# Kernel tuning notes

Measured on AMD Instinct MI355X. Metric: run time of the kernel, lower is better.

The kernel has to match this reference:

```python
import jax, jax.numpy as jnp
import numpy as np

L, D, H = 4, 1024, 16
HD = D // H
VOCAB = 100000
EPS = 1e-5


def layernorm(x, g, b):
    mu = jnp.mean(x, axis=-1, keepdims=True)
    var = jnp.var(x, axis=-1, keepdims=True)
    return (x - mu) * jax.lax.rsqrt(var + EPS) * g + b


def setup_inputs() -> dict:
    key = jax.random.key(0)
    ks = jax.random.split(key, 12)
    s = 0.02
    return {
        "input_ids": jax.random.randint(ks[0], (8, 512), 0, VOCAB),
        "encoder_state": jax.random.normal(ks[1], (8, 1024, D), dtype=jnp.float32),
        "cross_attn_mask": jnp.zeros((8, 1, 1, 1024), dtype=jnp.float32),
        "emb": jax.random.normal(ks[2], (VOCAB, D), dtype=jnp.float32) * s,
        "ln_g": jnp.ones((L, D), dtype=jnp.float32),
        "ln_b": jnp.zeros((L, D), dtype=jnp.float32),
        "wq": jax.random.normal(ks[3], (L, D, D), dtype=jnp.float32) * s,
        "bq": jnp.zeros((L, D), dtype=jnp.float32),
        "wk": jax.random.normal(ks[4], (L, D, D), dtype=jnp.float32) * s,
        "bk": jnp.zeros((L, D), dtype=jnp.float32),
        "wv": jax.random.normal(ks[5], (L, D, D), dtype=jnp.float32) * s,
        "bv": jnp.zeros((L, D), dtype=jnp.float32),
    }


def reference(input_ids, encoder_state, cross_attn_mask, emb, ln_g, ln_b, wq, bq, wk, bk, wv, bv):
    N, Tq = input_ids.shape
    Tk = encoder_state.shape[1]
    scale = 1.0 / (HD ** 0.5)
    x = emb[input_ids]  # [N, Tq, D]; dropout is identity at eval
    for i in range(L):
        h = layernorm(x, ln_g[i], ln_b[i])
        q = (h @ wq[i] + bq[i]).reshape(N, Tq, H, HD)
        k = (encoder_state @ wk[i] + bk[i]).reshape(N, Tk, H, HD)
        v = (encoder_state @ wv[i] + bv[i]).reshape(N, Tk, H, HD)
        logits = jnp.einsum("bqhd,bkhd->bhqk", q, k) * scale + cross_attn_mask
        w = jax.nn.softmax(logits, axis=-1)
        x = jnp.einsum("bhqk,bkhd->bqhd", w, v).reshape(N, Tq, D)
        # note: no residual connection in the original layer
    return x
```

## Files before the change

### kernel.cpp

```cpp
#include <hip/hip_runtime.h>
#include <hip/hip_bf16.h>


typedef __attribute__((ext_vector_type(8))) short   bf16x8;
typedef __attribute__((ext_vector_type(8))) __bf16  bf16x8v;
typedef __attribute__((ext_vector_type(4))) short   s16x4;
typedef __attribute__((ext_vector_type(4))) float   f32x4;

__device__ inline short bf16s(float f) {
  __hip_bfloat16 h = __float2bfloat16(f);
  return *reinterpret_cast<short*>(&h);
}

__device__ inline f32x4 mfma16x16x32(bf16x8 a, bf16x8 b, f32x4 c) {
  return __builtin_amdgcn_mfma_f32_16x16x32_bf16(
      __builtin_bit_cast(bf16x8v, a), __builtin_bit_cast(bf16x8v, b), c, 0, 0, 0);
}

__global__ __launch_bounds__(256) void conv_bf16_kernel(const float* __restrict__ in,
                                                        short* __restrict__ out) {
  int i = (blockIdx.x * 256 + threadIdx.x) * 4;
  float4 v = *reinterpret_cast<const float4*>(in + i);
  s16x4 o; o.x = bf16s(v.x); o.y = bf16s(v.y); o.z = bf16s(v.z); o.w = bf16s(v.w);
  *reinterpret_cast<s16x4*>(out + i) = o;
}

__global__ __launch_bounds__(256) void transpose_w_kernel(
    const float* __restrict__ wq, const float* __restrict__ wk, const float* __restrict__ wv,
    short* __restrict__ wqT, short* __restrict__ wkvT) {
  int mat = blockIdx.z;
  const float* src; short* dst;
  if (mat < 4)      { src = wq + (long)mat * 1048576;       dst = wqT  + (long)mat * 1048576; }
  else if (mat < 8) { src = wk + (long)(mat - 4) * 1048576; dst = wkvT + (long)(mat - 4) * 2097152; }
  else              { src = wv + (long)(mat - 8) * 1048576; dst = wkvT + (long)(mat - 8) * 2097152 + 1048576; }
  __shared__ float t[32][33];
  int tx = threadIdx.x, ty = threadIdx.y;
  int x0 = blockIdx.x * 32, y0 = blockIdx.y * 32;
  #pragma unroll
  for (int j = 0; j < 32; j += 8)
    t[ty + j][tx] = src[(long)(y0 + ty + j) * 1024 + x0 + tx];
  __syncthreads();
  #pragma unroll
  for (int j = 0; j < 32; j += 8)
    dst[(long)(x0 + ty + j) * 1024 + y0 + tx] = bf16s(t[tx][ty + j]);
}

__global__ __launch_bounds__(256) void gather_kernel(const int* __restrict__ ids,
                                                     const float* __restrict__ emb,
                                                     float* __restrict__ x) {
  int row = blockIdx.x;
  long id = ids[row];
  float4 v = reinterpret_cast<const float4*>(emb + id * 1024)[threadIdx.x];
  reinterpret_cast<float4*>(x + (long)row * 1024)[threadIdx.x] = v;
}

__global__ __launch_bounds__(256) void ln_kernel(const float* __restrict__ x,
                                                 const float* __restrict__ g,
                                                 const float* __restrict__ b,
                                                 short* __restrict__ h) {
  int row = blockIdx.x, t = threadIdx.x;
  float4 v = reinterpret_cast<const float4*>(x + (long)row * 1024)[t];
  float s  = v.x + v.y + v.z + v.w;
  float sq = v.x * v.x + v.y * v.y + v.z * v.z + v.w * v.w;
  #pragma unroll
  for (int m = 32; m >= 1; m >>= 1) { s += __shfl_xor(s, m); sq += __shfl_xor(sq, m); }
  __shared__ float red[8];
  int w = t >> 6;
  if ((t & 63) == 0) { red[w * 2] = s; red[w * 2 + 1] = sq; }
  __syncthreads();
  s  = red[0] + red[2] + red[4] + red[6];
  sq = red[1] + red[3] + red[5] + red[7];
  float mu  = s * 0.0009765625f;
  float var = sq * 0.0009765625f - mu * mu;
  float rs  = rsqrtf(var + 1e-5f);
  float4 gg = reinterpret_cast<const float4*>(g)[t];
  float4 bb = reinterpret_cast<const float4*>(b)[t];
  s16x4 o;
  o.x = bf16s((v.x - mu) * rs * gg.x + bb.x);
  o.y = bf16s((v.y - mu) * rs * gg.y + bb.y);
  o.z = bf16s((v.z - mu) * rs * gg.z + bb.z);
  o.w = bf16s((v.w - mu) * rs * gg.w + bb.w);
  reinterpret_cast<s16x4*>(h + (long)row * 1024)[t] = o;
}

template <int KV>
__global__ __launch_bounds__(256, 2) void gemm_kernel(
    const short* __restrict__ A, const short* __restrict__ WT,
    const float* __restrict__ bias0, const float* __restrict__ bias1,
    short* __restrict__ out0, short* __restrict__ out1) {
  __shared__ union {
    struct { short a[128 * 64]; short b[128 * 64]; } s;
    short c[4][64 * 72];
  } lds;

  const int t = threadIdx.x;
  const int lane = t & 63, w = t >> 6;
  const int lo = lane & 15, hi = lane >> 4;
  const int wr = w >> 1, wc = w & 1;
  const long bm0 = (long)blockIdx.x * 128, bn0 = (long)blockIdx.y * 128;

  f32x4 acc[4][4] = {};

  const int srow = t >> 3;
  const int sc = t & 7;

  for (int kt = 0; kt < 16; ++kt) {
    __syncthreads();
    #pragma unroll
    for (int p = 0; p < 4; ++p) {
      const int row = p * 32 + srow;
      const int cs = sc ^ (row & 7);
      __builtin_amdgcn_global_load_lds(
          (const __attribute__((address_space(1))) void*)(A + (bm0 + row) * 1024 + kt * 64 + cs * 8),
          (__attribute__((address_space(3))) void*)&lds.s.a[row * 64 + sc * 8], 16, 0, 0);
      __builtin_amdgcn_global_load_lds(
          (const __attribute__((address_space(1))) void*)(WT + (bn0 + row) * 1024 + kt * 64 + cs * 8),
          (__attribute__((address_space(3))) void*)&lds.s.b[row * 64 + sc * 8], 16, 0, 0);
    }
    __syncthreads();
    #pragma unroll
    for (int kk = 0; kk < 2; ++kk) {
      bf16x8 af[4], bfr[4];
      #pragma unroll
      for (int i = 0; i < 4; ++i) {
        const int ar = wr * 64 + i * 16 + lo;
        af[i] = *reinterpret_cast<const bf16x8*>(
            &lds.s.a[ar * 64 + (((kk * 4 + hi) ^ (ar & 7)) * 8)]);
        const int br = wc * 64 + i * 16 + lo;
        bfr[i] = *reinterpret_cast<const bf16x8*>(
            &lds.s.b[br * 64 + (((kk * 4 + hi) ^ (br & 7)) * 8)]);
      }
      #pragma unroll
      for (int i = 0; i < 4; ++i)
        #pragma unroll
        for (int j = 0; j < 4; ++j)
          acc[i][j] = mfma16x16x32(af[i], bfr[j], acc[i][j]);
    }
  }

  const bool vpath = KV && (bn0 >= 1024);
  float bval[4];
  #pragma unroll
  for (int j = 0; j < 4; ++j) {
    const int col = (int)bn0 + wc * 64 + j * 16 + lo;
    bval[j] = vpath ? bias1[col - 1024] : bias0[col];
  }

  if (vpath) {
    const int bidx = (int)(bm0 >> 10);
    const int tk0  = (int)(bm0 & 1023);
    #pragma unroll
    for (int i = 0; i < 4; ++i) {
      const int tok = tk0 + wr * 64 + i * 16 + 4 * hi;
      #pragma unroll
      for (int j = 0; j < 4; ++j) {
        const int dfull = (int)bn0 - 1024 + wc * 64 + j * 16 + lo;
        s16x4 pk;
        #pragma unroll
        for (int r = 0; r < 4; ++r) pk[r] = bf16s(acc[i][j][r] + bval[j]);
        *reinterpret_cast<s16x4*>(out1 + ((long)(bidx * 1024 + dfull)) * 1024 + tok) = pk;
      }
    }
  } else {
    __syncthreads();
    #pragma unroll
    for (int i = 0; i < 4; ++i)
      #pragma unroll
      for (int j = 0; j < 4; ++j)
        #pragma unroll
        for (int r = 0; r < 4; ++r)
          lds.c[w][(i * 16 + 4 * hi + r) * 72 + j * 16 + lo] = bf16s(acc[i][j][r] + bval[j]);
    asm volatile("s_waitcnt lgkmcnt(0)" ::: "memory");
    #pragma unroll
    for (int ps = 0; ps < 8; ++ps) {
      const int rr = ps * 8 + (lane >> 3);
      const int cc = (lane & 7) * 8;
      bf16x8 vv = *reinterpret_cast<const bf16x8*>(&lds.c[w][rr * 72 + cc]);
      *reinterpret_cast<bf16x8*>(out0 + (bm0 + wr * 64 + rr) * 1024 + bn0 + wc * 64 + cc) = vv;
    }
  }
}

__global__ __launch_bounds__(256) void attn_kernel(
    const short* __restrict__ qbuf, const short* __restrict__ kbuf,
    const short* __restrict__ vT, const float* __restrict__ mask,
    float* __restrict__ dst) {
  __shared__ short pl[4][16 * 40];
  const int b = blockIdx.x >> 4, h = blockIdx.x & 15;
  const int t = threadIdx.x, w = t >> 6, lane = t & 63;
  const int lo = lane & 15, hi = lane >> 4;
  const int q0 = blockIdx.y * 64 + w * 16;

  const short* qrow = qbuf + (long)(b * 512 + q0 + lo) * 1024 + h * 64;
  const bf16x8 aq0 = *reinterpret_cast<const bf16x8*>(qrow + hi * 8);
  const bf16x8 aq1 = *reinterpret_cast<const bf16x8*>(qrow + 32 + hi * 8);

  f32x4 o[4] = {};
  float m_r[4] = {-1e30f, -1e30f, -1e30f, -1e30f};
  float l_r[4] = {};
  const float scale = 0.125f;
  const float* mrow = mask + b * 1024;
  short* plw = pl[w];

  for (int kb = 0; kb < 32; ++kb) {
    const short* kbase = kbuf + (long)(b * 1024 + kb * 32) * 1024 + h * 64;
    bf16x8 b00 = *reinterpret_cast<const bf16x8*>(kbase + (long)lo * 1024 + hi * 8);
    bf16x8 b01 = *reinterpret_cast<const bf16x8*>(kbase + (long)lo * 1024 + 32 + hi * 8);
    bf16x8 b10 = *reinterpret_cast<const bf16x8*>(kbase + (long)(16 + lo) * 1024 + hi * 8);
    bf16x8 b11 = *reinterpret_cast<const bf16x8*>(kbase + (long)(16 + lo) * 1024 + 32 + hi * 8);
    f32x4 z = {0.f, 0.f, 0.f, 0.f};
    f32x4 s0 = mfma16x16x32(aq0, b00, z);
    s0 = mfma16x16x32(aq1, b01, s0);
    f32x4 s1 = mfma16x16x32(aq0, b10, z);
    s1 = mfma16x16x32(aq1, b11, s1);

    const float mk0 = mrow[kb * 32 + lo];
    const float mk1 = mrow[kb * 32 + 16 + lo];

    float p0[4], p1[4], lm[4];
    #pragma unroll
    for (int r = 0; r < 4; ++r) {
      p0[r] = s0[r] * scale + mk0;
      p1[r] = s1[r] * scale + mk1;
      lm[r] = fmaxf(p0[r], p1[r]);
    }
    #pragma unroll
    for (int mm = 1; mm <= 8; mm <<= 1)
      #pragma unroll
      for (int r = 0; r < 4; ++r) lm[r] = fmaxf(lm[r], __shfl_xor(lm[r], mm));

    float alpha[4], ts[4];
    #pragma unroll
    for (int r = 0; r < 4; ++r) {
      const float mn = fmaxf(m_r[r], lm[r]);
      alpha[r] = __expf(m_r[r] - mn);
      m_r[r] = mn;
      p0[r] = __expf(p0[r] - mn);
      p1[r] = __expf(p1[r] - mn);
      ts[r] = p0[r] + p1[r];
    }
    #pragma unroll
    for (int mm = 1; mm <= 8; mm <<= 1)
      #pragma unroll
      for (int r = 0; r < 4; ++r) ts[r] += __shfl_xor(ts[r], mm);

    #pragma unroll
    for (int r = 0; r < 4; ++r) {
      l_r[r] = l_r[r] * alpha[r] + ts[r];
      o[0][r] *= alpha[r]; o[1][r] *= alpha[r]; o[2][r] *= alpha[r]; o[3][r] *= alpha[r];
      plw[(4 * hi + r) * 40 + lo]      = bf16s(p0[r]);
      plw[(4 * hi + r) * 40 + 16 + lo] = bf16s(p1[r]);
    }
    asm volatile("s_waitcnt lgkmcnt(0)" ::: "memory");
    const bf16x8 pa = *reinterpret_cast<const bf16x8*>(&plw[lo * 40 + hi * 8]);
    const short* vbase = vT + ((long)(b * 1024 + h * 64)) * 1024 + kb * 32;
    #pragma unroll
    for (int nd = 0; nd < 4; ++nd) {
      bf16x8 bv = *reinterpret_cast<const bf16x8*>(vbase + (long)(nd * 16 + lo) * 1024 + hi * 8);
      o[nd] = mfma16x16x32(pa, bv, o[nd]);
    }
  }

  #pragma unroll
  for (int r = 0; r < 4; ++r) {
    const float invl = 1.0f / l_r[r];
    float* drow = dst + (long)(b * 512 + q0 + 4 * hi + r) * 1024 + h * 64;
    #pragma unroll
    for (int nd = 0; nd < 4; ++nd) drow[nd * 16 + lo] = o[nd][r] * invl;
  }
}

extern "C" void kernel_launch(void* const* d_in, const int* in_sizes, int n_in,
                              void* d_out, int out_size, void* d_ws, size_t ws_size,
                              hipStream_t stream) {
  const int*   ids  = (const int*)d_in[0];
  const float* enc  = (const float*)d_in[1];
  const float* mask = (const float*)d_in[2];
  const float* emb  = (const float*)d_in[3];
  const float* ln_g = (const float*)d_in[4];
  const float* ln_b = (const float*)d_in[5];
  const float* wq   = (const float*)d_in[6];
  const float* bq   = (const float*)d_in[7];
  const float* wk   = (const float*)d_in[8];
  const float* bk   = (const float*)d_in[9];
  const float* wv   = (const float*)d_in[10];
  const float* bv   = (const float*)d_in[11];
  float* out = (float*)d_out;

  char* ws = (char*)d_ws;
  short* encB = (short*)ws; ws += (long)8192 * 1024 * 2;
  short* wqT  = (short*)ws; ws += (long)4 * 1024 * 1024 * 2;
  short* wkvT = (short*)ws; ws += (long)4 * 2048 * 1024 * 2;
  float* xbuf = (float*)ws; ws += (long)4096 * 1024 * 4;
  short* hbuf = (short*)ws; ws += (long)4096 * 1024 * 2;
  short* qbuf = (short*)ws; ws += (long)4096 * 1024 * 2;
  short* kbuf = (short*)ws; ws += (long)8192 * 1024 * 2;
  short* vT   = (short*)ws; ws += (long)8192 * 1024 * 2;

  conv_bf16_kernel<<<8192, 256, 0, stream>>>(enc, encB);
  transpose_w_kernel<<<dim3(32, 32, 12), dim3(32, 8), 0, stream>>>(wq, wk, wv, wqT, wkvT);
  gather_kernel<<<4096, 256, 0, stream>>>(ids, emb, xbuf);

  for (int i = 0; i < 4; ++i) {
    ln_kernel<<<4096, 256, 0, stream>>>(xbuf, ln_g + i * 1024, ln_b + i * 1024, hbuf);
    gemm_kernel<0><<<dim3(32, 8), 256, 0, stream>>>(
        hbuf, wqT + (long)i * 1024 * 1024, bq + i * 1024, nullptr, qbuf, nullptr);
    gemm_kernel<1><<<dim3(64, 16), 256, 0, stream>>>(
        encB, wkvT + (long)i * 2048 * 1024, bk + i * 1024, bv + i * 1024, kbuf, vT);
    float* dst = (i == 3) ? out : xbuf;
    attn_kernel<<<dim3(128, 8), 256, 0, stream>>>(qbuf, kbuf, vT, mask, dst);
  }
}
```

Baseline: 1.225 ms.

## Batch all-layer KV projections into one GEMM and widen attention key blocks

The K/V projections do not depend on the layer chain, so all four layers' K and V are now computed in a single large GEMM launch before the loop and kept in per-layer workspace buffers. The attention kernel processes 64 keys per iteration instead of 32, uses a swizzled LDS layout for the probability tile, and skips rescaling when the running max grows by 8 or less. MFMA sections are also wrapped in s_setprio. This removes three small GEMM launches and makes each one fill the GPU better, at the cost of four times the K/V workspace memory. The skipped rescale lets unnormalized exponentials reach up to e^8, which bf16 and fp32 can hold.

```diff
diff --git a/kernel.cpp b/kernel.cpp
--- a/kernel.cpp
+++ b/kernel.cpp
@@ -97,7 +97,11 @@
   const int lane = t & 63, w = t >> 6;
   const int lo = lane & 15, hi = lane >> 4;
   const int wr = w >> 1, wc = w & 1;
-  const long bm0 = (long)blockIdx.x * 128, bn0 = (long)blockIdx.y * 128;
+  const long bm0 = (long)blockIdx.x * 128;
+  const long bn0g = (long)blockIdx.y * 128;
+  const int  layer = KV ? (int)(bn0g >> 11) : 0;
+  const long bn0 = KV ? (bn0g & 2047) : bn0g;
+  const short* WTl = KV ? WT + (long)layer * 2097152 : WT;
 
   f32x4 acc[4][4] = {};
 
@@ -114,7 +118,7 @@
           (const __attribute__((address_space(1))) void*)(A + (bm0 + row) * 1024 + kt * 64 + cs * 8),
           (__attribute__((address_space(3))) void*)&lds.s.a[row * 64 + sc * 8], 16, 0, 0);
       __builtin_amdgcn_global_load_lds(
-          (const __attribute__((address_space(1))) void*)(WT + (bn0 + row) * 1024 + kt * 64 + cs * 8),
+          (const __attribute__((address_space(1))) void*)(WTl + (bn0 + row) * 1024 + kt * 64 + cs * 8),
           (__attribute__((address_space(3))) void*)&lds.s.b[row * 64 + sc * 8], 16, 0, 0);
     }
     __syncthreads();
@@ -130,11 +134,13 @@
         bfr[i] = *reinterpret_cast<const bf16x8*>(
             &lds.s.b[br * 64 + (((kk * 4 + hi) ^ (br & 7)) * 8)]);
       }
+      __builtin_amdgcn_s_setprio(1);
       #pragma unroll
       for (int i = 0; i < 4; ++i)
         #pragma unroll
         for (int j = 0; j < 4; ++j)
           acc[i][j] = mfma16x16x32(af[i], bfr[j], acc[i][j]);
+      __builtin_amdgcn_s_setprio(0);
     }
   }
 
@@ -143,8 +149,10 @@
   #pragma unroll
   for (int j = 0; j < 4; ++j) {
     const int col = (int)bn0 + wc * 64 + j * 16 + lo;
-    bval[j] = vpath ? bias1[col - 1024] : bias0[col];
-  }
+    bval[j] = KV ? (vpath ? bias1[layer * 1024 + col - 1024] : bias0[layer * 1024 + col])
+                 : bias0[col];
+  }
+  const long lofs = (long)layer * 8388608;
 
   if (vpath) {
     const int bidx = (int)(bm0 >> 10);
@@ -158,7 +166,7 @@
         s16x4 pk;
         #pragma unroll
         for (int r = 0; r < 4; ++r) pk[r] = bf16s(acc[i][j][r] + bval[j]);
-        *reinterpret_cast<s16x4*>(out1 + ((long)(bidx * 1024 + dfull)) * 1024 + tok) = pk;
+        *reinterpret_cast<s16x4*>(out1 + lofs + ((long)(bidx * 1024 + dfull)) * 1024 + tok) = pk;
       }
     }
   } else {
@@ -176,7 +184,7 @@
       const int rr = ps * 8 + (lane >> 3);
       const int cc = (lane & 7) * 8;
       bf16x8 vv = *reinterpret_cast<const bf16x8*>(&lds.c[w][rr * 72 + cc]);
-      *reinterpret_cast<bf16x8*>(out0 + (bm0 + wr * 64 + rr) * 1024 + bn0 + wc * 64 + cc) = vv;
+      *reinterpret_cast<bf16x8*>(out0 + lofs + (bm0 + wr * 64 + rr) * 1024 + bn0 + wc * 64 + cc) = vv;
     }
   }
 }
@@ -185,7 +193,7 @@
     const short* __restrict__ qbuf, const short* __restrict__ kbuf,
     const short* __restrict__ vT, const float* __restrict__ mask,
     float* __restrict__ dst) {
-  __shared__ short pl[4][16 * 40];
+  __shared__ short pl[4][16 * 64];
   const int b = blockIdx.x >> 4, h = blockIdx.x & 15;
   const int t = threadIdx.x, w = t >> 6, lane = t & 63;
   const int lo = lane & 15, hi = lane >> 4;
@@ -200,65 +208,93 @@
   float l_r[4] = {};
   const float scale = 0.125f;
   const float* mrow = mask + b * 1024;
-  short* plw = pl[w];
-
-  for (int kb = 0; kb < 32; ++kb) {
-    const short* kbase = kbuf + (long)(b * 1024 + kb * 32) * 1024 + h * 64;
-    bf16x8 b00 = *reinterpret_cast<const bf16x8*>(kbase + (long)lo * 1024 + hi * 8);
-    bf16x8 b01 = *reinterpret_cast<const bf16x8*>(kbase + (long)lo * 1024 + 32 + hi * 8);
-    bf16x8 b10 = *reinterpret_cast<const bf16x8*>(kbase + (long)(16 + lo) * 1024 + hi * 8);
-    bf16x8 b11 = *reinterpret_cast<const bf16x8*>(kbase + (long)(16 + lo) * 1024 + 32 + hi * 8);
-    f32x4 z = {0.f, 0.f, 0.f, 0.f};
-    f32x4 s0 = mfma16x16x32(aq0, b00, z);
-    s0 = mfma16x16x32(aq1, b01, s0);
-    f32x4 s1 = mfma16x16x32(aq0, b10, z);
-    s1 = mfma16x16x32(aq1, b11, s1);
-
-    const float mk0 = mrow[kb * 32 + lo];
-    const float mk1 = mrow[kb * 32 + 16 + lo];
-
-    float p0[4], p1[4], lm[4];
+  char* plw = (char*)pl[w];
+
+  for (int kb = 0; kb < 16; ++kb) {
+    const short* kbase = kbuf + (long)(b * 1024 + kb * 64) * 1024 + h * 64;
+    f32x4 s[4];
+    __builtin_amdgcn_s_setprio(1);
+    #pragma unroll
+    for (int kt = 0; kt < 4; ++kt) {
+      bf16x8 k0 = *reinterpret_cast<const bf16x8*>(kbase + (long)(kt * 16 + lo) * 1024 + hi * 8);
+      bf16x8 k1 = *reinterpret_cast<const bf16x8*>(kbase + (long)(kt * 16 + lo) * 1024 + 32 + hi * 8);
+      f32x4 z = {0.f, 0.f, 0.f, 0.f};
+      s[kt] = mfma16x16x32(aq0, k0, z);
+      s[kt] = mfma16x16x32(aq1, k1, s[kt]);
+    }
+    __builtin_amdgcn_s_setprio(0);
+
+    float mk[4];
+    #pragma unroll
+    for (int kt = 0; kt < 4; ++kt) mk[kt] = mrow[kb * 64 + kt * 16 + lo];
+
+    float p[4][4], lm[4];
     #pragma unroll
     for (int r = 0; r < 4; ++r) {
-      p0[r] = s0[r] * scale + mk0;
-      p1[r] = s1[r] * scale + mk1;
-      lm[r] = fmaxf(p0[r], p1[r]);
+      p[0][r] = s[0][r] * scale + mk[0];
+      p[1][r] = s[1][r] * scale + mk[1];
+      p[2][r] = s[2][r] * scale + mk[2];
+      p[3][r] = s[3][r] * scale + mk[3];
+      lm[r] = fmaxf(fmaxf(p[0][r], p[1][r]), fmaxf(p[2][r], p[3][r]));
     }
     #pragma unroll
     for (int mm = 1; mm <= 8; mm <<= 1)
       #pragma unroll
       for (int r = 0; r < 4; ++r) lm[r] = fmaxf(lm[r], __shfl_xor(lm[r], mm));
 
-    float alpha[4], ts[4];
+    bool need = false;
+    #pragma unroll
+    for (int r = 0; r < 4; ++r) need = need || (lm[r] > m_r[r] + 8.0f);
+    if (need) {
+      #pragma unroll
+      for (int r = 0; r < 4; ++r) {
+        const float mn = fmaxf(m_r[r], lm[r]);
+        const float al = __expf(m_r[r] - mn);
+        m_r[r] = mn;
+        l_r[r] *= al;
+        o[0][r] *= al; o[1][r] *= al; o[2][r] *= al; o[3][r] *= al;
+      }
+    }
+
+    float ts[4];
     #pragma unroll
     for (int r = 0; r < 4; ++r) {
-      const float mn = fmaxf(m_r[r], lm[r]);
-      alpha[r] = __expf(m_r[r] - mn);
-      m_r[r] = mn;
-      p0[r] = __expf(p0[r] - mn);
-      p1[r] = __expf(p1[r] - mn);
-      ts[r] = p0[r] + p1[r];
+      p[0][r] = __expf(p[0][r] - m_r[r]);
+      p[1][r] = __expf(p[1][r] - m_r[r]);
+      p[2][r] = __expf(p[2][r] - m_r[r]);
+      p[3][r] = __expf(p[3][r] - m_r[r]);
+      ts[r] = (p[0][r] + p[1][r]) + (p[2][r] + p[3][r]);
     }
     #pragma unroll
     for (int mm = 1; mm <= 8; mm <<= 1)
       #pragma unroll
       for (int r = 0; r < 4; ++r) ts[r] += __shfl_xor(ts[r], mm);
-
-    #pragma unroll
-    for (int r = 0; r < 4; ++r) {
-      l_r[r] = l_r[r] * alpha[r] + ts[r];
-      o[0][r] *= alpha[r]; o[1][r] *= alpha[r]; o[2][r] *= alpha[r]; o[3][r] *= alpha[r];
-      plw[(4 * hi + r) * 40 + lo]      = bf16s(p0[r]);
-      plw[(4 * hi + r) * 40 + 16 + lo] = bf16s(p1[r]);
-    }
+    #pragma unroll
+    for (int r = 0; r < 4; ++r) l_r[r] += ts[r];
+
+    #pragma unroll
+    for (int kt = 0; kt < 4; ++kt)
+      #pragma unroll
+      for (int r = 0; r < 4; ++r) {
+        const int row = 4 * hi + r;
+        const int byte = (row * 128 + (kt * 16 + lo) * 2) ^ ((row & 7) << 4);
+        *reinterpret_cast<short*>(plw + byte) = bf16s(p[kt][r]);
+      }
     asm volatile("s_waitcnt lgkmcnt(0)" ::: "memory");
-    const bf16x8 pa = *reinterpret_cast<const bf16x8*>(&plw[lo * 40 + hi * 8]);
-    const short* vbase = vT + ((long)(b * 1024 + h * 64)) * 1024 + kb * 32;
+    const int rb = (lo * 128 + hi * 16) ^ ((lo & 7) << 4);
+    const bf16x8 pa0 = *reinterpret_cast<const bf16x8*>(plw + rb);
+    const bf16x8 pa1 = *reinterpret_cast<const bf16x8*>(plw + (rb ^ 64));
+
+    const short* vbase = vT + ((long)(b * 1024 + h * 64)) * 1024 + kb * 64;
+    __builtin_amdgcn_s_setprio(1);
     #pragma unroll
     for (int nd = 0; nd < 4; ++nd) {
-      bf16x8 bv = *reinterpret_cast<const bf16x8*>(vbase + (long)(nd * 16 + lo) * 1024 + hi * 8);
-      o[nd] = mfma16x16x32(pa, bv, o[nd]);
-    }
+      bf16x8 v0 = *reinterpret_cast<const bf16x8*>(vbase + (long)(nd * 16 + lo) * 1024 + hi * 8);
+      bf16x8 v1 = *reinterpret_cast<const bf16x8*>(vbase + (long)(nd * 16 + lo) * 1024 + 32 + hi * 8);
+      o[nd] = mfma16x16x32(pa0, v0, o[nd]);
+      o[nd] = mfma16x16x32(pa1, v1, o[nd]);
+    }
+    __builtin_amdgcn_s_setprio(0);
   }
 
   #pragma unroll
@@ -288,26 +324,28 @@
   float* out = (float*)d_out;
 
   char* ws = (char*)d_ws;
-  short* encB = (short*)ws; ws += (long)8192 * 1024 * 2;
-  short* wqT  = (short*)ws; ws += (long)4 * 1024 * 1024 * 2;
-  short* wkvT = (short*)ws; ws += (long)4 * 2048 * 1024 * 2;
-  float* xbuf = (float*)ws; ws += (long)4096 * 1024 * 4;
-  short* hbuf = (short*)ws; ws += (long)4096 * 1024 * 2;
-  short* qbuf = (short*)ws; ws += (long)4096 * 1024 * 2;
-  short* kbuf = (short*)ws; ws += (long)8192 * 1024 * 2;
-  short* vT   = (short*)ws; ws += (long)8192 * 1024 * 2;
+  short* encB  = (short*)ws; ws += (long)8192 * 1024 * 2;
+  short* wqT   = (short*)ws; ws += (long)4 * 1024 * 1024 * 2;
+  short* wkvT  = (short*)ws; ws += (long)4 * 2048 * 1024 * 2;
+  float* xbuf  = (float*)ws; ws += (long)4096 * 1024 * 4;
+  short* hbuf  = (short*)ws; ws += (long)4096 * 1024 * 2;
+  short* qbuf  = (short*)ws; ws += (long)4096 * 1024 * 2;
+  short* kbuf4 = (short*)ws; ws += (long)4 * 8192 * 1024 * 2;
+  short* vT4   = (short*)ws; ws += (long)4 * 8192 * 1024 * 2;
 
   conv_bf16_kernel<<<8192, 256, 0, stream>>>(enc, encB);
   transpose_w_kernel<<<dim3(32, 32, 12), dim3(32, 8), 0, stream>>>(wq, wk, wv, wqT, wkvT);
   gather_kernel<<<4096, 256, 0, stream>>>(ids, emb, xbuf);
+
+  gemm_kernel<1><<<dim3(64, 64), 256, 0, stream>>>(
+      encB, wkvT, bk, bv, kbuf4, vT4);
 
   for (int i = 0; i < 4; ++i) {
     ln_kernel<<<4096, 256, 0, stream>>>(xbuf, ln_g + i * 1024, ln_b + i * 1024, hbuf);
     gemm_kernel<0><<<dim3(32, 8), 256, 0, stream>>>(
         hbuf, wqT + (long)i * 1024 * 1024, bq + i * 1024, nullptr, qbuf, nullptr);
-    gemm_kernel<1><<<dim3(64, 16), 256, 0, stream>>>(
-        encB, wkvT + (long)i * 2048 * 1024, bk + i * 1024, bv + i * 1024, kbuf, vT);
     float* dst = (i == 3) ? out : xbuf;
-    attn_kernel<<<dim3(128, 8), 256, 0, stream>>>(qbuf, kbuf, vT, mask, dst);
-  }
-}
+    attn_kernel<<<dim3(128, 8), 256, 0, stream>>>(
+        qbuf, kbuf4 + (long)i * 8388608, vT4 + (long)i * 8388608, mask, dst);
+  }
+}
```

New measurement: 1.214 ms. About the same (-0.8%).
